# Performance work log

Hardware: AMD Instinct MI355X
Metric: run time of the kernel (lower is better)

Reference implementation:

```python
import jax, jax.numpy as jnp
import numpy as np

USER_NUM = 100000
ITEM_NUM = 50000
N = USER_NUM + ITEM_NUM
D = 64
NNZ = 2400000
B = 4096
NLEVEL = 3
LEAF = 32
HID = 256
NCLS = 2
NLAYERS = 2
EPS = 0.1
TAU = 0.2


def _l2norm(x, axis=-1):
    return x / jnp.clip(jnp.linalg.norm(x, axis=axis, keepdims=True), 1e-12)


def setup_inputs():
    key = jax.random.key(0)
    ks = jax.random.split(key, 32)
    def w(k, shape):
        fan = shape[-2] if len(shape) >= 2 else shape[-1]
        return jax.random.normal(k, shape, jnp.float32) / np.sqrt(fan)
    z = lambda *s: jnp.zeros(s, jnp.float32)
    return {
        "ego_emb": w(ks[0], (N, D)),
        "gc_w": w(ks[1], (NLAYERS, D, D)), "gc_b": z(NLAYERS, D),
        "bi_w": w(ks[2], (NLAYERS, D, D)), "bi_b": z(NLAYERS, D),
        "uh_w": w(ks[3], (NLEVEL, D, D)), "uh_b": z(NLEVEL, D),
        "ih_w": w(ks[4], (NLEVEL, D, D)), "ih_b": z(NLEVEL, D),
        "ud_w1": w(ks[5], (NLEVEL, D, HID)), "ud_b1": z(NLEVEL, HID),
        "ud_w2": w(ks[6], (NLEVEL, HID, LEAF)), "ud_b2": z(NLEVEL, LEAF),
        "id_w1": w(ks[7], (NLEVEL, D, HID)), "id_b1": z(NLEVEL, HID),
        "id_w2": w(ks[8], (NLEVEL, HID, LEAF)), "id_b2": z(NLEVEL, LEAF),
        "q_w": w(ks[9], (LEAF, LEAF)), "q_b": z(LEAF),
        "k_w": w(ks[10], (LEAF, LEAF)), "k_b": z(LEAF),
        "v_w": w(ks[11], (LEAF, LEAF)), "v_b": z(LEAF),
        "dg_w1": w(ks[12], (NLEVEL * LEAF, D)), "dg_b1": z(D),
        "dg_w2": w(ks[13], (D, D)), "dg_b2": z(D),
        "pr_w": w(ks[14], (D, NCLS)), "pr_b": z(NCLS),
        "adj_vals": jax.random.uniform(ks[15], (NNZ,), jnp.float32) / 16.0,
        "hier_skills": jax.random.uniform(ks[16], (B, NLEVEL * LEAF), jnp.float32),
        "user_id": jax.random.randint(ks[17], (B,), 0, USER_NUM),
        "item_id": jax.random.randint(ks[18], (B,), 0, ITEM_NUM),
        "adj_rows": jax.random.randint(ks[19], (NNZ,), 0, N),
        "adj_cols": jax.random.randint(ks[20], (NNZ,), 0, N),
    }


def _sam(x, q_w, q_b, k_w, k_b, v_w, v_b):
    # x: [B, S, d], single-head self-attention (n_heads=1)
    d = x.shape[-1]
    q = x @ q_w + q_b
    k = x @ k_w + k_b
    v = x @ v_w + v_b
    scores = jnp.einsum('bsd,btd->bst', q, k) / jnp.sqrt(jnp.float32(d))
    attn = jax.nn.softmax(scores, axis=-1)  # softmax over key axis t
    return jnp.einsum('bst,btd->bsd', attn, v)


def _cl_loss(v1, v2):
    n1 = _l2norm(v1)
    n2 = _l2norm(v2)
    pos = jnp.exp(jnp.sum(n1 * n2, -1) / TAU)
    ttl = jnp.sum(jnp.exp(n1 @ n2.T / TAU), axis=1)
    return jnp.mean(-jnp.log(pos / ttl))


def _cl_module(recs, key):
    # recs: [L, B, LEAF]
    noise = jax.random.uniform(key, recs.shape, recs.dtype)
    recs_new = recs + jnp.sign(recs) * _l2norm(noise) * EPS
    return jnp.mean(jax.vmap(_cl_loss)(recs, recs_new))


def reference(ego_emb, gc_w, gc_b, bi_w, bi_b, uh_w, uh_b, ih_w, ih_b,
              ud_w1, ud_b1, ud_w2, ud_b2, id_w1, id_b1, id_w2, id_b2,
              q_w, q_b, k_w, k_b, v_w, v_b, dg_w1, dg_b1, dg_w2, dg_b2,
              pr_w, pr_b, adj_vals, hier_skills, user_id, item_id,
              adj_rows, adj_cols):
    # ---- NGCF propagation: sparse adj matmul + bi-interaction ----
    E = ego_emb
    E_sum = ego_emb
    for l in range(NLAYERS):
        side = jax.ops.segment_sum(adj_vals[:, None] * E[adj_cols], adj_rows,
                                   num_segments=N)  # spmm(adj_norm, E)
        sum_e = jax.nn.leaky_relu(side @ gc_w[l] + gc_b[l])
        bi_e = jax.nn.leaky_relu((E * side) @ bi_w[l] + bi_b[l])
        E = _l2norm(sum_e + bi_e)  # dropout -> identity (eval)
        E_sum = E_sum + E
    ue = E_sum[:USER_NUM][user_id]   # [B, D]
    ie = E_sum[USER_NUM:][item_id]   # [B, D]
    # ---- hierarchy projections + disentangled encoders (stacked over levels) ----
    u_reps = jnp.tanh(jnp.einsum('bd,lde->lbe', ue, uh_w) + uh_b[:, None, :])
    i_reps = jnp.tanh(jnp.einsum('bd,lde->lbe', ie, ih_w) + ih_b[:, None, :])
    u_recs = jnp.einsum('lbh,lhk->lbk',
                        jnp.tanh(jnp.einsum('lbd,ldh->lbh', u_reps, ud_w1) + ud_b1[:, None, :]),
                        ud_w2) + ud_b2[:, None, :]  # [L, B, LEAF]
    i_recs = jnp.einsum('lbh,lhk->lbk',
                        jnp.tanh(jnp.einsum('lbd,ldh->lbh', i_reps, id_w1) + id_b1[:, None, :]),
                        id_w2) + id_b2[:, None, :]
    # ---- self-attention across levels ----
    u_att = _sam(u_recs.transpose(1, 0, 2), q_w, q_b, k_w, k_b, v_w, v_b)  # [B, L, LEAF]
    i_att = _sam(i_recs.transpose(1, 0, 2), q_w, q_b, k_w, k_b, v_w, v_b)
    # ---- contrastive losses (detached in original via torch.Tensor(...)) ----
    kc = jax.random.split(jax.random.key(42), 2)
    cl = _cl_module(u_att.transpose(1, 0, 2), kc[0]) + _cl_module(i_att.transpose(1, 0, 2), kc[1])
    cl = jax.lax.stop_gradient(cl)
    # ---- diagnosis head ----
    skills = hier_skills.reshape(B, NLEVEL, LEAF)
    diag = ((jax.nn.sigmoid(u_att) - jax.nn.sigmoid(i_att)) * skills).reshape(B, NLEVEL * LEAF)
    h = jnp.tanh(diag @ dg_w1 + dg_b1) @ dg_w2 + dg_b2  # dropout -> identity (eval)
    out = jax.nn.softmax(h @ pr_w + pr_b, axis=-1)
    return (out, cl)
```

## Files before the change

### kernel.cpp

```cpp
#include <hip/hip_runtime.h>
#include <stdint.h>
#include <math.h>

#define USER_N 100000
#define NODE_N 150000
#define DD 64
#define NNZE 2400000
#define BB 4096
#define NLV 3
#define LF 32
#define HALF_SZ 196608u
#define NTILE 586
#define NSUB 8
#define SCAP 1024
#define EPB 4096
#define LCAP 5120

typedef __attribute__((ext_vector_type(8))) short bf16x8;
typedef __attribute__((ext_vector_type(4))) float f32x4;
typedef __attribute__((ext_vector_type(2))) float f32x2;

#define XCC_ID_IMM 63508

__host__ __device__ inline void tf_block(uint32_t k0, uint32_t k1, uint32_t& x0, uint32_t& x1) {
  uint32_t ks[3] = {k0, k1, k0 ^ k1 ^ 0x1BD11BDAu};
  x0 += ks[0]; x1 += ks[1];
  const int R0[4] = {13, 15, 26, 6};
  const int R1[4] = {17, 29, 16, 24};
#pragma unroll
  for (int i = 0; i < 5; ++i) {
    const int* R = (i & 1) ? R1 : R0;
#pragma unroll
    for (int j = 0; j < 4; ++j) {
      x0 += x1;
      x1 = (x1 << R[j]) | (x1 >> (32 - R[j]));
      x1 ^= x0;
    }
    x0 += ks[(i + 1) % 3];
    x1 += ks[(i + 2) % 3] + (uint32_t)(i + 1);
  }
}

__device__ inline float tf_uniform(uint32_t ka, uint32_t kb, uint32_t m) {
  uint32_t x0, x1;
  bool first = m < HALF_SZ;
  if (first) { x0 = m; x1 = m + HALF_SZ; } else { x0 = m - HALF_SZ; x1 = m; }
  tf_block(ka, kb, x0, x1);
  uint32_t bits = first ? x0 : x1;
  return __uint_as_float((bits >> 9) | 0x3f800000u) - 1.0f;
}

__device__ inline unsigned short f2bf(float x) {
  uint32_t b = __float_as_uint(x);
  return (unsigned short)((b + 0x7FFFu + ((b >> 16) & 1u)) >> 16);
}

__device__ inline unsigned char f2fp8(float x) {
  return (unsigned char)(__builtin_amdgcn_cvt_pk_fp8_f32(x, x, 0, false) & 0xFF);
}

__device__ inline void fp8_fma(float4& acc, uint2 rec, uint32_t wrd) {
  float vv = __uint_as_float(rec.y);
  f32x2 lo = __builtin_amdgcn_cvt_pk_f32_fp8((int)wrd, false);
  f32x2 hi = __builtin_amdgcn_cvt_pk_f32_fp8((int)wrd, true);
  acc.x = fmaf(vv, lo.x, acc.x);
  acc.y = fmaf(vv, lo.y, acc.y);
  acc.z = fmaf(vv, hi.x, acc.z);
  acc.w = fmaf(vv, hi.y, acc.w);
}

__global__ __launch_bounds__(256) void k_init(
    const float* __restrict__ ego, uint32_t* __restrict__ E8,
    const float* __restrict__ uh_w, const float* __restrict__ ud_w1,
    const float* __restrict__ ud_w2, const float* __restrict__ ih_w,
    const float* __restrict__ id_w1, const float* __restrict__ id_w2,
    unsigned short* __restrict__ s1t, unsigned short* __restrict__ s2t,
    unsigned short* __restrict__ s3t) {
  if (blockIdx.x < 9375) {
    int i = blockIdx.x * 256 + threadIdx.x;
    float4 v = ((const float4*)ego)[i];
    int w01 = __builtin_amdgcn_cvt_pk_fp8_f32(v.x, v.y, 0, false);
    int w = __builtin_amdgcn_cvt_pk_fp8_f32(v.z, v.w, w01, true);
    E8[i] = (uint32_t)w;
    return;
  }
  int i = (blockIdx.x - 9375) * 256 + threadIdx.x;
  if (i < 24576) {
    int sl = i >> 12, r = i & 4095, e = r >> 6, d = r & 63;
    const float* src = (sl >= 3 ? ih_w : uh_w);
    int l = sl % 3;
    s1t[i] = f2bf(src[l * 4096 + d * 64 + e]);
  } else if (i < 24576 + 98304) {
    int j = i - 24576;
    int sl = j >> 14, r = j & 16383, e = r >> 6, d = r & 63;
    const float* src = (sl >= 3 ? id_w1 : ud_w1);
    int l = sl % 3;
    s2t[j] = f2bf(src[l * 16384 + d * 256 + e]);
  } else if (i < 172032) {
    int j = i - 24576 - 98304;
    int sl = j >> 13, r = j & 8191, e = r >> 8, d = r & 255;
    const float* src = (sl >= 3 ? id_w2 : ud_w2);
    int l = sl % 3;
    s3t[j] = f2bf(src[l * 8192 + d * 32 + e]);
  }
}

__global__ __launch_bounds__(256) void k_scatter_t(const int* __restrict__ rows,
                                                   const int* __restrict__ cols,
                                                   const float* __restrict__ vals,
                                                   int* __restrict__ cursor,
                                                   uint2* __restrict__ sedge_r) {
  __shared__ int cnt[NTILE];
  __shared__ int curs[NTILE];
  int t = threadIdx.x;
  for (int i = t; i < NTILE; i += 256) cnt[i] = 0;
  __syncthreads();
  int r[16];
  int ebase = blockIdx.x * EPB;
#pragma unroll
  for (int j = 0; j < 16; ++j) {
    int e = ebase + j * 256 + t;
    r[j] = (e < NNZE) ? rows[e] : -1;
    if (r[j] >= 0) atomicAdd(&cnt[r[j] >> 8], 1);
  }
  __syncthreads();
  unsigned myx = __builtin_amdgcn_s_getreg(XCC_ID_IMM) & (NSUB - 1);
  for (int i = t; i < NTILE; i += 256) {
    int c = cnt[i];
    curs[i] = c ? atomicAdd(&cursor[(i * NSUB + (int)myx) * 16], c) : 0;
  }
  __syncthreads();
#pragma unroll
  for (int j = 0; j < 16; ++j) {
    if (r[j] < 0) continue;
    int e = ebase + j * 256 + t;
    int tile = r[j] >> 8;
    uint2 rec = make_uint2((uint32_t)cols[e] | ((uint32_t)(r[j] & 255) << 18),
                           __float_as_uint(vals[e]));
    int p = atomicAdd(&curs[tile], 1);
    if (p < SCAP) {
      sedge_r[(size_t)(tile * NSUB + (int)myx) * SCAP + p] = rec;
    } else {
#pragma unroll 1
      for (int att = 1; att < NSUB; ++att) {
        int seg = tile * NSUB + (int)((myx + att) & (NSUB - 1));
        int p2 = atomicAdd(&cursor[seg * 16], 1);
        if (p2 < SCAP) { sedge_r[(size_t)seg * SCAP + p2] = rec; break; }
      }
    }
  }
}

__global__ __launch_bounds__(256) void k_sort_t(const uint2* __restrict__ sedge_r,
                                                const int* __restrict__ cursor,
                                                uint2* __restrict__ sedge,
                                                int* __restrict__ row_start) {
  __shared__ int hist[256], buf[256], curs[256];
  __shared__ int obase_s;
  __shared__ uint2 staged[LCAP];
  int t = threadIdx.x;
  int tile = blockIdx.x;
  if (t == 0) obase_s = 0;
  hist[t] = 0;
  __syncthreads();
  int ob = 0;
  for (int i = t; i < tile * NSUB; i += 256) {
    int c = cursor[i * 16];
    ob += (c < SCAP) ? c : SCAP;
  }
  if (ob) atomicAdd(&obase_s, ob);
  int segcnt[NSUB];
#pragma unroll
  for (int x = 0; x < NSUB; ++x) {
    int c = cursor[(tile * NSUB + x) * 16];
    segcnt[x] = (c < SCAP) ? c : SCAP;
  }
#pragma unroll 1
  for (int x = 0; x < NSUB; ++x) {
    const uint2* sp = sedge_r + (size_t)(tile * NSUB + x) * SCAP;
    for (int i = t; i < segcnt[x]; i += 256)
      atomicAdd(&hist[sp[i].x >> 18], 1);
  }
  __syncthreads();
  int obase = obase_s;
  int v = hist[t];
  buf[t] = v;
  __syncthreads();
  for (int off = 1; off < 256; off <<= 1) {
    int add = (t >= off) ? buf[t - off] : 0;
    __syncthreads();
    buf[t] += add;
    __syncthreads();
  }
  int total = buf[255];
  int excl = buf[t] - v;
  curs[t] = excl;
  int row = tile * 256 + t;
  if (row < NODE_N) row_start[row] = obase + excl;
  if (tile == NTILE - 1 && t == 0) row_start[NODE_N] = NNZE;
  __syncthreads();
#pragma unroll 1
  for (int x = 0; x < NSUB; ++x) {
    const uint2* sp = sedge_r + (size_t)(tile * NSUB + x) * SCAP;
    for (int i = t; i < segcnt[x]; i += 256) {
      uint2 rec = sp[i];
      int rl = rec.x >> 18;
      int p = atomicAdd(&curs[rl], 1);
      uint2 outrec = make_uint2(rec.x & 0x3FFFFu, rec.y);
      if (p < LCAP) staged[p] = outrec;
      else sedge[obase + p] = outrec;
    }
  }
  __syncthreads();
  int n = (total < LCAP) ? total : LCAP;
  for (int i = t; i < n; i += 256)
    sedge[obase + i] = staged[i];
}

__global__ __launch_bounds__(256) void k_spmm(const uint32_t* __restrict__ E8,
                                              const uint2* __restrict__ sedge,
                                              const int* __restrict__ row_start,
                                              unsigned short* __restrict__ side16,
                                              unsigned short* __restrict__ p16) {
  int r = blockIdx.x * 4 + (threadIdx.x >> 6);
  int lane = threadIdx.x & 63;
  int g = lane >> 4;
  int q = lane & 15;
  int rs = row_start[r], re = row_start[r + 1];
  float4 acc = make_float4(0.f, 0.f, 0.f, 0.f);
  int e = rs;
  for (; e + 16 <= re; e += 16) {
    uint2 e0 = sedge[e + g];
    uint2 e1 = sedge[e + 4 + g];
    uint2 e2 = sedge[e + 8 + g];
    uint2 e3 = sedge[e + 12 + g];
    uint32_t a0 = E8[(size_t)e0.x * 16 + q];
    uint32_t a1 = E8[(size_t)e1.x * 16 + q];
    uint32_t a2 = E8[(size_t)e2.x * 16 + q];
    uint32_t a3 = E8[(size_t)e3.x * 16 + q];
    fp8_fma(acc, e0, a0);
    fp8_fma(acc, e1, a1);
    fp8_fma(acc, e2, a2);
    fp8_fma(acc, e3, a3);
  }
  for (; e + 8 <= re; e += 8) {
    uint2 e0 = sedge[e + g];
    uint2 e1 = sedge[e + 4 + g];
    uint32_t a0 = E8[(size_t)e0.x * 16 + q];
    uint32_t a1 = E8[(size_t)e1.x * 16 + q];
    fp8_fma(acc, e0, a0);
    fp8_fma(acc, e1, a1);
  }
  for (; e + 4 <= re; e += 4) {
    uint2 e0 = sedge[e + g];
    uint32_t a0 = E8[(size_t)e0.x * 16 + q];
    fp8_fma(acc, e0, a0);
  }
  for (; e < re; ++e) {
    if (g == (e & 3)) {
      uint2 e0 = sedge[e];
      uint32_t a0 = E8[(size_t)e0.x * 16 + q];
      fp8_fma(acc, e0, a0);
    }
  }
#pragma unroll
  for (int off = 16; off <= 32; off <<= 1) {
    acc.x += __shfl_xor(acc.x, off, 64);
    acc.y += __shfl_xor(acc.y, off, 64);
    acc.z += __shfl_xor(acc.z, off, 64);
    acc.w += __shfl_xor(acc.w, off, 64);
  }
  if (g == 0) {
    uint32_t ew = E8[(size_t)r * 16 + q];
    f32x2 elo = __builtin_amdgcn_cvt_pk_f32_fp8((int)ew, false);
    f32x2 ehi = __builtin_amdgcn_cvt_pk_f32_fp8((int)ew, true);
    ushort4 s16, pp;
    s16.x = f2bf(acc.x); s16.y = f2bf(acc.y); s16.z = f2bf(acc.z); s16.w = f2bf(acc.w);
    pp.x = f2bf(acc.x * elo.x); pp.y = f2bf(acc.y * elo.y);
    pp.z = f2bf(acc.z * ehi.x); pp.w = f2bf(acc.w * ehi.y);
    *(ushort4*)&side16[(size_t)r * DD + q * 4] = s16;
    *(ushort4*)&p16[(size_t)r * DD + q * 4] = pp;
  }
}

__global__ __launch_bounds__(256) void k_transform(const float* __restrict__ gw,
                                                   const float* __restrict__ gb,
                                                   const float* __restrict__ bw,
                                                   const float* __restrict__ bb,
                                                   const unsigned short* __restrict__ side16,
                                                   const unsigned short* __restrict__ p16,
                                                   float* __restrict__ Eout,
                                                   unsigned char* __restrict__ E8b) {
  int t = threadIdx.x;
  int wv = t >> 6, lane = t & 63;
  int n = lane & 15, quad = lane >> 4;
  bf16x8 wg[4][2], wb[4][2];
  float gbl[4], bbl[4];
#pragma unroll
  for (int c = 0; c < 4; ++c) {
    gbl[c] = gb[c * 16 + n];
    bbl[c] = bb[c * 16 + n];
#pragma unroll
    for (int h = 0; h < 2; ++h) {
#pragma unroll
      for (int j = 0; j < 8; ++j) {
        int k = h * 32 + quad * 8 + j;
        wg[c][h][j] = (short)f2bf(gw[k * 64 + c * 16 + n]);
        wb[c][h][j] = (short)f2bf(bw[k * 64 + c * 16 + n]);
      }
    }
  }
  const f32x4 z = {0.f, 0.f, 0.f, 0.f};
  for (int tile = blockIdx.x * 4 + wv; tile < NODE_N / 16; tile += gridDim.x * 4) {
    int i0 = tile * 16;
    bf16x8 as0 = *(const bf16x8*)&side16[(size_t)(i0 + n) * DD + quad * 8];
    bf16x8 as1 = *(const bf16x8*)&side16[(size_t)(i0 + n) * DD + 32 + quad * 8];
    bf16x8 ap0 = *(const bf16x8*)&p16[(size_t)(i0 + n) * DD + quad * 8];
    bf16x8 ap1 = *(const bf16x8*)&p16[(size_t)(i0 + n) * DD + 32 + quad * 8];
    float v[4][4];
    float sq0 = 0.f, sq1 = 0.f, sq2 = 0.f, sq3 = 0.f;
#pragma unroll
    for (int c = 0; c < 4; ++c) {
      f32x4 ag = __builtin_amdgcn_mfma_f32_16x16x32_bf16(as0, wg[c][0], z, 0, 0, 0);
      ag = __builtin_amdgcn_mfma_f32_16x16x32_bf16(as1, wg[c][1], ag, 0, 0, 0);
      f32x4 ab = __builtin_amdgcn_mfma_f32_16x16x32_bf16(ap0, wb[c][0], z, 0, 0, 0);
      ab = __builtin_amdgcn_mfma_f32_16x16x32_bf16(ap1, wb[c][1], ab, 0, 0, 0);
#pragma unroll
      for (int r = 0; r < 4; ++r) {
        float a1 = ag[r] + gbl[c];
        a1 = (a1 > 0.f) ? a1 : 0.01f * a1;
        float a2 = ab[r] + bbl[c];
        a2 = (a2 > 0.f) ? a2 : 0.01f * a2;
        float vv = a1 + a2;
        v[c][r] = vv;
        if (r == 0) sq0 += vv * vv;
        else if (r == 1) sq1 += vv * vv;
        else if (r == 2) sq2 += vv * vv;
        else sq3 += vv * vv;
      }
    }
#pragma unroll
    for (int off = 1; off < 16; off <<= 1) {
      sq0 += __shfl_xor(sq0, off, 64);
      sq1 += __shfl_xor(sq1, off, 64);
      sq2 += __shfl_xor(sq2, off, 64);
      sq3 += __shfl_xor(sq3, off, 64);
    }
    float inv0 = 1.f / fmaxf(sqrtf(sq0), 1e-12f);
    float inv1 = 1.f / fmaxf(sqrtf(sq1), 1e-12f);
    float inv2 = 1.f / fmaxf(sqrtf(sq2), 1e-12f);
    float inv3 = 1.f / fmaxf(sqrtf(sq3), 1e-12f);
#pragma unroll
    for (int c = 0; c < 4; ++c) {
      float vn0 = v[c][0] * inv0;
      float vn1 = v[c][1] * inv1;
      float vn2 = v[c][2] * inv2;
      float vn3 = v[c][3] * inv3;
      size_t o0 = (size_t)(i0 + quad * 4 + 0) * DD + c * 16 + n;
      size_t o1 = o0 + DD, o2 = o1 + DD, o3 = o2 + DD;
      Eout[o0] = vn0; Eout[o1] = vn1; Eout[o2] = vn2; Eout[o3] = vn3;
      E8b[o0] = f2fp8(vn0); E8b[o1] = f2fp8(vn1);
      E8b[o2] = f2fp8(vn2); E8b[o3] = f2fp8(vn3);
    }
  }
}

__global__ __launch_bounds__(128) void k_gather(const float* __restrict__ ego,
                                                const float* __restrict__ E1,
                                                const float* __restrict__ E2,
                                                const int* __restrict__ uid,
                                                const int* __restrict__ iid,
                                                unsigned short* __restrict__ ue16,
                                                unsigned short* __restrict__ ie16) {
  int b = blockIdx.x, t = threadIdx.x;
  if (t < 64) {
    size_t o = (size_t)uid[b] * 64 + t;
    ue16[(size_t)b * 64 + t] = f2bf(ego[o] + E1[o] + E2[o]);
  } else {
    int d = t - 64;
    size_t o = (size_t)(USER_N + iid[b]) * 64 + d;
    ie16[(size_t)b * 64 + d] = f2bf(ego[o] + E1[o] + E2[o]);
  }
}

__global__ __launch_bounds__(256) void k_encoder5(
    const unsigned short* __restrict__ ue16, const unsigned short* __restrict__ ie16,
    const unsigned short* __restrict__ s1t, const unsigned short* __restrict__ s2t,
    const unsigned short* __restrict__ s3t,
    const float* __restrict__ uh_b, const float* __restrict__ ud_b1,
    const float* __restrict__ ud_b2, const float* __restrict__ ih_b,
    const float* __restrict__ id_b1, const float* __restrict__ id_b2,
    float* __restrict__ recs_u, float* __restrict__ recs_i) {
  __shared__ unsigned short R1[32][64];
  __shared__ unsigned short T[32][256];
  int t = threadIdx.x;
  int w = t >> 6, lane = t & 63;
  int n = lane & 15, quad = lane >> 4;
  int trow = w & 1;
  int cg = w >> 1;
  int r0 = blockIdx.x * 32;
  int l = blockIdx.y, side = blockIdx.z;
  int sl = side * 3 + l;
  const unsigned short* x16 = side ? ie16 : ue16;
  const float* hb = side ? ih_b : uh_b;
  const float* bb1 = side ? id_b1 : ud_b1;
  const float* bb2 = side ? id_b2 : ud_b2;
  float* recs = side ? recs_i : recs_u;
  const f32x4 z = {0.f, 0.f, 0.f, 0.f};

  {
    const unsigned short* xr = &x16[(size_t)(r0 + trow * 16 + n) * 64];
    bf16x8 a0 = *(const bf16x8*)&xr[quad * 8];
    bf16x8 a1 = *(const bf16x8*)&xr[32 + quad * 8];
    const unsigned short* Wt = s1t + (size_t)sl * 4096;
#pragma unroll
    for (int cc = 0; cc < 2; ++cc) {
      int cb = cg * 2 + cc;
      bf16x8 wb0 = *(const bf16x8*)&Wt[(size_t)(cb * 16 + n) * 64 + quad * 8];
      bf16x8 wb1 = *(const bf16x8*)&Wt[(size_t)(cb * 16 + n) * 64 + 32 + quad * 8];
      f32x4 acc = __builtin_amdgcn_mfma_f32_16x16x32_bf16(a0, wb0, z, 0, 0, 0);
      acc = __builtin_amdgcn_mfma_f32_16x16x32_bf16(a1, wb1, acc, 0, 0, 0);
      float bias = hb[l * 64 + cb * 16 + n];
#pragma unroll
      for (int r = 0; r < 4; ++r)
        R1[trow * 16 + quad * 4 + r][cb * 16 + n] = f2bf(tanhf(acc[r] + bias));
    }
  }
  __syncthreads();

  {
    bf16x8 a0 = *(const bf16x8*)&R1[trow * 16 + n][quad * 8];
    bf16x8 a1 = *(const bf16x8*)&R1[trow * 16 + n][32 + quad * 8];
    const unsigned short* Wt = s2t + (size_t)sl * 16384;
#pragma unroll
    for (int cc = 0; cc < 8; ++cc) {
      int cb = cg * 8 + cc;
      bf16x8 wb0 = *(const bf16x8*)&Wt[(size_t)(cb * 16 + n) * 64 + quad * 8];
      bf16x8 wb1 = *(const bf16x8*)&Wt[(size_t)(cb * 16 + n) * 64 + 32 + quad * 8];
      f32x4 acc = __builtin_amdgcn_mfma_f32_16x16x32_bf16(a0, wb0, z, 0, 0, 0);
      acc = __builtin_amdgcn_mfma_f32_16x16x32_bf16(a1, wb1, acc, 0, 0, 0);
      float bias = bb1[l * 256 + cb * 16 + n];
#pragma unroll
      for (int r = 0; r < 4; ++r)
        T[trow * 16 + quad * 4 + r][cb * 16 + n] = f2bf(tanhf(acc[r] + bias));
    }
  }
  __syncthreads();

  {
    const unsigned short* Wt = s3t + (size_t)sl * 8192;
    f32x4 acc = z;
#pragma unroll
    for (int h = 0; h < 8; ++h) {
      bf16x8 a = *(const bf16x8*)&T[trow * 16 + n][h * 32 + quad * 8];
      bf16x8 b = *(const bf16x8*)&Wt[(size_t)(cg * 16 + n) * 256 + h * 32 + quad * 8];
      acc = __builtin_amdgcn_mfma_f32_16x16x32_bf16(a, b, acc, 0, 0, 0);
    }
    float bias = bb2[l * 32 + cg * 16 + n];
#pragma unroll
    for (int r = 0; r < 4; ++r)
      recs[((size_t)l * BB + (r0 + trow * 16 + quad * 4 + r)) * 32 + cg * 16 + n] =
          acc[r] + bias;
  }
}

__global__ __launch_bounds__(256) void k_attn(const float* __restrict__ recs_u,
                                              const float* __restrict__ recs_i,
                                              const float* __restrict__ qw, const float* __restrict__ qb,
                                              const float* __restrict__ kw, const float* __restrict__ kb,
                                              const float* __restrict__ vw, const float* __restrict__ vb,
                                              float* __restrict__ att_u,
                                              float* __restrict__ att_i) {
  const float* recs = blockIdx.y ? recs_i : recs_u;
  float* att = blockIdx.y ? att_i : att_u;
  int t = threadIdx.x;
  int b = blockIdx.x * 8 + (t >> 5);
  int d = t & 31;
  float x0 = recs[((size_t)0 * BB + b) * 32 + d];
  float x1 = recs[((size_t)1 * BB + b) * 32 + d];
  float x2 = recs[((size_t)2 * BB + b) * 32 + d];
  float q0 = qb[d], q1 = q0, q2 = q0;
  float c0 = kb[d], c1 = c0, c2 = c0;
  float v0 = vb[d], v1 = v0, v2 = v0;
#pragma unroll 4
  for (int kk = 0; kk < 32; ++kk) {
    float xa = __shfl(x0, kk, 32);
    float xb = __shfl(x1, kk, 32);
    float xc = __shfl(x2, kk, 32);
    float wq = qw[kk * 32 + d], wk = kw[kk * 32 + d], wv = vw[kk * 32 + d];
    q0 += xa * wq; q1 += xb * wq; q2 += xc * wq;
    c0 += xa * wk; c1 += xb * wk; c2 += xc * wk;
    v0 += xa * wv; v1 += xb * wv; v2 += xc * wv;
  }
  float qs[3] = {q0, q1, q2}, ks[3] = {c0, c1, c2}, vs[3] = {v0, v1, v2};
  float sc[3][3];
#pragma unroll
  for (int s = 0; s < 3; ++s)
#pragma unroll
    for (int u = 0; u < 3; ++u) {
      float p = qs[s] * ks[u];
#pragma unroll
      for (int off = 16; off; off >>= 1) p += __shfl_xor(p, off, 32);
      sc[s][u] = p * 0.17677669529663687f;
    }
#pragma unroll
  for (int s = 0; s < 3; ++s) {
    float m = fmaxf(sc[s][0], fmaxf(sc[s][1], sc[s][2]));
    float e0 = __expf(sc[s][0] - m), e1 = __expf(sc[s][1] - m), e2 = __expf(sc[s][2] - m);
    float inv = 1.f / (e0 + e1 + e2);
    att[(size_t)b * 96 + s * 32 + d] = (e0 * vs[0] + e1 * vs[1] + e2 * vs[2]) * inv;
  }
}

__global__ __launch_bounds__(256) void k_noise(const float* __restrict__ att_u,
                                               const float* __restrict__ att_i,
                                               uint32_t ku0, uint32_t ku1, uint32_t ki0, uint32_t ki1,
                                               unsigned short* __restrict__ n1b,
                                               unsigned short* __restrict__ n2b,
                                               float* __restrict__ posdot) {
  int t = threadIdx.x;
  int g = blockIdx.x * 8 + (t >> 5);
  int k = t & 31;
  int side = g / (NLV * BB);
  int rem = g - side * (NLV * BB);
  int l = rem >> 12;
  int b = rem & 4095;
  const float* att = side ? att_i : att_u;
  uint32_t ka = side ? ki0 : ku0;
  uint32_t kb = side ? ki1 : ku1;
  float r = att[(size_t)b * 96 + l * 32 + k];
  float ss = r * r;
#pragma unroll
  for (int off = 16; off; off >>= 1) ss += __shfl_xor(ss, off, 32);
  float v1 = r / fmaxf(sqrtf(ss), 1e-12f);
  uint32_t m = ((uint32_t)(l * BB + b)) * 32u + (uint32_t)k;
  float u = tf_uniform(ka, kb, m);
  float us = u * u;
#pragma unroll
  for (int off = 16; off; off >>= 1) us += __shfl_xor(us, off, 32);
  float un = u / fmaxf(sqrtf(us), 1e-12f);
  float sgn = (r > 0.f) ? 1.f : ((r < 0.f) ? -1.f : 0.f);
  float rn = r + sgn * un * 0.1f;
  float s2 = rn * rn;
#pragma unroll
  for (int off = 16; off; off >>= 1) s2 += __shfl_xor(s2, off, 32);
  float v2 = rn / fmaxf(sqrtf(s2), 1e-12f);
  float pd = v1 * v2;
#pragma unroll
  for (int off = 16; off; off >>= 1) pd += __shfl_xor(pd, off, 32);
  size_t o = (size_t)g * 32 + k;
  n1b[o] = f2bf(v1);
  n2b[o] = f2bf(v2);
  if (k == 0) posdot[g] = pd;
}

__global__ __launch_bounds__(256) void k_ttl(const unsigned short* __restrict__ n1b,
                                             const unsigned short* __restrict__ n2b,
                                             float* __restrict__ ttl) {
  int t = threadIdx.x;
  int wv = t >> 6, lane = t & 63;
  int sl = blockIdx.x >> 6;
  int istripe = blockIdx.x & 63;
  int i0 = istripe * 64 + wv * 16;
  const unsigned short* ab = n1b + (size_t)sl * BB * 32;
  const unsigned short* bb = n2b + (size_t)sl * BB * 32;
  int m = lane & 15, quad = lane >> 4;
  bf16x8 afrag = *(const bf16x8*)&ab[(size_t)(i0 + m) * 32 + quad * 8];
  float r0a = 0.f, r1a = 0.f, r2a = 0.f, r3a = 0.f;
  f32x4 z = {0.f, 0.f, 0.f, 0.f};
  for (int jt = 0; jt < 256; jt += 4) {
    bf16x8 b0 = *(const bf16x8*)&bb[((size_t)((jt + 0) * 16 + m)) * 32 + quad * 8];
    bf16x8 b1 = *(const bf16x8*)&bb[((size_t)((jt + 1) * 16 + m)) * 32 + quad * 8];
    bf16x8 b2 = *(const bf16x8*)&bb[((size_t)((jt + 2) * 16 + m)) * 32 + quad * 8];
    bf16x8 b3 = *(const bf16x8*)&bb[((size_t)((jt + 3) * 16 + m)) * 32 + quad * 8];
    f32x4 s0 = __builtin_amdgcn_mfma_f32_16x16x32_bf16(afrag, b0, z, 0, 0, 0);
    f32x4 s1 = __builtin_amdgcn_mfma_f32_16x16x32_bf16(afrag, b1, z, 0, 0, 0);
    f32x4 s2 = __builtin_amdgcn_mfma_f32_16x16x32_bf16(afrag, b2, z, 0, 0, 0);
    f32x4 s3 = __builtin_amdgcn_mfma_f32_16x16x32_bf16(afrag, b3, z, 0, 0, 0);
    r0a += __expf(s0.x * 5.f) + __expf(s1.x * 5.f) + __expf(s2.x * 5.f) + __expf(s3.x * 5.f);
    r1a += __expf(s0.y * 5.f) + __expf(s1.y * 5.f) + __expf(s2.y * 5.f) + __expf(s3.y * 5.f);
    r2a += __expf(s0.z * 5.f) + __expf(s1.z * 5.f) + __expf(s2.z * 5.f) + __expf(s3.z * 5.f);
    r3a += __expf(s0.w * 5.f) + __expf(s1.w * 5.f) + __expf(s2.w * 5.f) + __expf(s3.w * 5.f);
  }
#pragma unroll
  for (int off = 1; off < 16; off <<= 1) {
    r0a += __shfl_xor(r0a, off, 64);
    r1a += __shfl_xor(r1a, off, 64);
    r2a += __shfl_xor(r2a, off, 64);
    r3a += __shfl_xor(r3a, off, 64);
  }
  if (m == 0) {
    int rbase = sl * BB + i0 + quad * 4;
    ttl[rbase + 0] = r0a;
    ttl[rbase + 1] = r1a;
    ttl[rbase + 2] = r2a;
    ttl[rbase + 3] = r3a;
  }
}

__global__ __launch_bounds__(1024) void k_clred(const float* __restrict__ ttl,
                                                const float* __restrict__ posdot,
                                                float* __restrict__ outp) {
  __shared__ float red[1024];
  int t = threadIdx.x;
  float a = 0.f;
  for (int idx = t; idx < 6 * BB; idx += 1024)
    a += logf(ttl[idx]) - posdot[idx] * 5.0f;
  red[t] = a;
  __syncthreads();
  for (int off = 512; off; off >>= 1) {
    if (t < off) red[t] += red[t + off];
    __syncthreads();
  }
  if (t == 0) outp[2 * BB] = red[0] * (1.f / 12288.f);
}

__global__ __launch_bounds__(256) void k_head(const float* __restrict__ att_u,
                                              const float* __restrict__ att_i,
                                              const float* __restrict__ skills,
                                              const float* __restrict__ w1, const float* __restrict__ b1,
                                              const float* __restrict__ w2, const float* __restrict__ b2,
                                              const float* __restrict__ pw, const float* __restrict__ pb,
                                              float* __restrict__ outp) {
  __shared__ float diag[4][96], t1[4][64];
  int t = threadIdx.x;
  int w = t >> 6, lane = t & 63;
  int b = blockIdx.x * 4 + w;
  for (int j = lane; j < 96; j += 64) {
    float su = 1.f / (1.f + __expf(-att_u[(size_t)b * 96 + j]));
    float si = 1.f / (1.f + __expf(-att_i[(size_t)b * 96 + j]));
    diag[w][j] = (su - si) * skills[(size_t)b * 96 + j];
  }
  __syncthreads();
  float a = b1[lane];
#pragma unroll 8
  for (int j = 0; j < 96; ++j) a += diag[w][j] * w1[j * 64 + lane];
  t1[w][lane] = tanhf(a);
  __syncthreads();
  float h = b2[lane];
#pragma unroll 8
  for (int kk = 0; kk < 64; ++kk) h += t1[w][kk] * w2[kk * 64 + lane];
  float p0 = h * pw[lane * 2 + 0];
  float p1 = h * pw[lane * 2 + 1];
#pragma unroll
  for (int off = 32; off; off >>= 1) {
    p0 += __shfl_xor(p0, off, 64);
    p1 += __shfl_xor(p1, off, 64);
  }
  if (lane == 0) {
    float l0 = p0 + pb[0], l1 = p1 + pb[1];
    float m = fmaxf(l0, l1);
    float e0 = __expf(l0 - m), e1 = __expf(l1 - m);
    float inv = 1.f / (e0 + e1);
    outp[(size_t)b * 2 + 0] = e0 * inv;
    outp[(size_t)b * 2 + 1] = e1 * inv;
  }
}

extern "C" void kernel_launch(void* const* d_in, const int* in_sizes, int n_in,
                              void* d_out, int out_size, void* d_ws, size_t ws_size,
                              hipStream_t stream) {
  const float* ego    = (const float*)d_in[0];
  const float* gc_w   = (const float*)d_in[1];
  const float* gc_b   = (const float*)d_in[2];
  const float* bi_w   = (const float*)d_in[3];
  const float* bi_b   = (const float*)d_in[4];
  const float* uh_w   = (const float*)d_in[5];
  const float* uh_b   = (const float*)d_in[6];
  const float* ih_w   = (const float*)d_in[7];
  const float* ih_b   = (const float*)d_in[8];
  const float* ud_w1  = (const float*)d_in[9];
  const float* ud_b1  = (const float*)d_in[10];
  const float* ud_w2  = (const float*)d_in[11];
  const float* ud_b2  = (const float*)d_in[12];
  const float* id_w1  = (const float*)d_in[13];
  const float* id_b1  = (const float*)d_in[14];
  const float* id_w2  = (const float*)d_in[15];
  const float* id_b2  = (const float*)d_in[16];
  const float* q_w    = (const float*)d_in[17];
  const float* q_b    = (const float*)d_in[18];
  const float* k_w    = (const float*)d_in[19];
  const float* k_b    = (const float*)d_in[20];
  const float* v_w    = (const float*)d_in[21];
  const float* v_b    = (const float*)d_in[22];
  const float* dg_w1  = (const float*)d_in[23];
  const float* dg_b1  = (const float*)d_in[24];
  const float* dg_w2  = (const float*)d_in[25];
  const float* dg_b2  = (const float*)d_in[26];
  const float* pr_w   = (const float*)d_in[27];
  const float* pr_b   = (const float*)d_in[28];
  const float* adj_vals = (const float*)d_in[29];
  const float* skills = (const float*)d_in[30];
  const int* user_id  = (const int*)d_in[31];
  const int* item_id  = (const int*)d_in[32];
  const int* adj_rows = (const int*)d_in[33];
  const int* adj_cols = (const int*)d_in[34];
  float* outp = (float*)d_out;

  char* w = (char*)d_ws;
  auto alloc = [&](size_t bytes) -> char* {
    char* p = w;
    w += (bytes + 255) & ~(size_t)255;
    return p;
  };
  float* E1     = (float*)alloc((size_t)NODE_N * DD * 4);
  float* E2     = (float*)alloc((size_t)NODE_N * DD * 4);
  uint32_t* E8  = (uint32_t*)alloc((size_t)NODE_N * DD);
  unsigned short* side16 = (unsigned short*)alloc((size_t)NODE_N * DD * 2);
  unsigned short* p16    = (unsigned short*)alloc((size_t)NODE_N * DD * 2);
  uint2* sedge_r= (uint2*)alloc((size_t)NTILE * NSUB * SCAP * 8);
  uint2* sedge  = (uint2*)alloc((size_t)NNZE * 8);
  int*   cursor = (int*)  alloc((size_t)NTILE * NSUB * 16 * 4);
  int*   row_start = (int*)alloc((size_t)(NODE_N + 1) * 4);
  float* posdot = (float*)alloc((size_t)6 * BB * 4);
  float* ttl    = (float*)alloc((size_t)6 * BB * 4);
  unsigned short* s1t = (unsigned short*)alloc((size_t)24576 * 2);
  unsigned short* s2t = (unsigned short*)alloc((size_t)98304 * 2);
  unsigned short* s3t = (unsigned short*)alloc((size_t)49152 * 2);

  char* ap = (char*)sedge_r;
  auto alias = [&](size_t bytes) -> char* {
    char* p = ap;
    ap += (bytes + 255) & ~(size_t)255;
    return p;
  };
  unsigned short* ue16 = (unsigned short*)alias((size_t)BB * 64 * 2);
  unsigned short* ie16 = (unsigned short*)alias((size_t)BB * 64 * 2);
  float* recs_u = (float*)alias((size_t)NLV * BB * 32 * 4);
  float* recs_i = (float*)alias((size_t)NLV * BB * 32 * 4);
  float* att_u  = (float*)alias((size_t)BB * 96 * 4);
  float* att_i  = (float*)alias((size_t)BB * 96 * 4);
  unsigned short* n1b = (unsigned short*)alias((size_t)6 * BB * 32 * 2);
  unsigned short* n2b = (unsigned short*)alias((size_t)6 * BB * 32 * 2);

  uint32_t a0 = 0, a1 = 2, b0 = 1, b1 = 3;
  tf_block(0u, 42u, a0, a1);
  tf_block(0u, 42u, b0, b1);
  uint32_t ku0 = a0, ku1 = b0;
  uint32_t ki0 = a1, ki1 = b1;

  (void)hipMemsetAsync(cursor, 0, (size_t)NTILE * NSUB * 16 * 4, stream);

  k_init<<<9375 + 672, 256, 0, stream>>>(ego, E8, uh_w, ud_w1, ud_w2,
                                         ih_w, id_w1, id_w2, s1t, s2t, s3t);
  k_scatter_t<<<(NNZE + EPB - 1) / EPB, 256, 0, stream>>>(adj_rows, adj_cols, adj_vals,
                                                          cursor, sedge_r);
  k_sort_t<<<NTILE, 256, 0, stream>>>(sedge_r, cursor, sedge, row_start);

  float* Ebufs[2] = {E1, E2};
  for (int l = 0; l < 2; ++l) {
    k_spmm<<<37500, 256, 0, stream>>>(E8, sedge, row_start, side16, p16);
    k_transform<<<1172, 256, 0, stream>>>(gc_w + l * 4096, gc_b + l * 64,
                                          bi_w + l * 4096, bi_b + l * 64,
                                          side16, p16, Ebufs[l], (unsigned char*)E8);
  }

  k_gather<<<4096, 128, 0, stream>>>(ego, E1, E2, user_id, item_id, ue16, ie16);

  dim3 ge(128, 3, 2);
  k_encoder5<<<ge, 256, 0, stream>>>(ue16, ie16, s1t, s2t, s3t,
                                     uh_b, ud_b1, ud_b2, ih_b, id_b1, id_b2,
                                     recs_u, recs_i);

  dim3 ga(512, 2);
  k_attn<<<ga, 256, 0, stream>>>(recs_u, recs_i, q_w, q_b, k_w, k_b, v_w, v_b,
                                 att_u, att_i);

  k_noise<<<3072, 256, 0, stream>>>(att_u, att_i, ku0, ku1, ki0, ki1, n1b, n2b, posdot);

  k_ttl<<<384, 256, 0, stream>>>(n1b, n2b, ttl);
  k_clred<<<1, 1024, 0, stream>>>(ttl, posdot, outp);

  k_head<<<1024, 256, 0, stream>>>(att_u, att_i, skills, dg_w1, dg_b1, dg_w2, dg_b2,
                                   pr_w, pr_b, outp);
}
```

Measured before the change: 540.6 us.

## Stage scatter records in LDS sorted by tile for coalesced global writes

The edge scatter kernel now ranks each edge within its tile bin during counting, builds an exclusive prefix sum of the bin counts in shared memory, and stages records contiguously per tile in LDS. It then writes the records out in bin order, so consecutive threads write consecutive addresses within each tile segment instead of scattering randomly. This aims to cut uncoalesced global stores, at the cost of about 40KB of LDS per block (lower occupancy) and an extra scan with several barriers.

```diff
diff --git a/kernel.cpp b/kernel.cpp
--- a/kernel.cpp
+++ b/kernel.cpp
@@ -111,23 +111,46 @@
                                                    int* __restrict__ cursor,
                                                    uint2* __restrict__ sedge_r) {
   __shared__ int cnt[NTILE];
-  __shared__ int curs[NTILE];
+  __shared__ int binbase[NTILE];
+  __shared__ int gbase[NTILE];
+  __shared__ int partial[256];
+  __shared__ uint2 staged[EPB];
+  __shared__ unsigned short tileof[EPB];
   int t = threadIdx.x;
   for (int i = t; i < NTILE; i += 256) cnt[i] = 0;
   __syncthreads();
-  int r[16];
   int ebase = blockIdx.x * EPB;
+  int r[16], rk[16];
 #pragma unroll
   for (int j = 0; j < 16; ++j) {
     int e = ebase + j * 256 + t;
     r[j] = (e < NNZE) ? rows[e] : -1;
-    if (r[j] >= 0) atomicAdd(&cnt[r[j] >> 8], 1);
-  }
-  __syncthreads();
+    rk[j] = (r[j] >= 0) ? atomicAdd(&cnt[r[j] >> 8], 1) : 0;
+  }
+  __syncthreads();
+  int b0 = t * 3;
+  int own = (b0 < NTILE) ? ((NTILE - b0 < 3) ? (NTILE - b0) : 3) : 0;
+  int s0 = 0;
+  for (int k = 0; k < own; ++k) s0 += cnt[b0 + k];
+  partial[t] = s0;
+  __syncthreads();
+  for (int off = 1; off < 256; off <<= 1) {
+    int add = (t >= off) ? partial[t - off] : 0;
+    __syncthreads();
+    partial[t] += add;
+    __syncthreads();
+  }
+  int excl = partial[t] - s0;
   unsigned myx = __builtin_amdgcn_s_getreg(XCC_ID_IMM) & (NSUB - 1);
-  for (int i = t; i < NTILE; i += 256) {
-    int c = cnt[i];
-    curs[i] = c ? atomicAdd(&cursor[(i * NSUB + (int)myx) * 16], c) : 0;
+  {
+    int run = excl;
+    for (int k = 0; k < own; ++k) {
+      int b = b0 + k;
+      int c = cnt[b];
+      binbase[b] = run;
+      gbase[b] = c ? atomicAdd(&cursor[(b * NSUB + (int)myx) * 16], c) : 0;
+      run += c;
+    }
   }
   __syncthreads();
 #pragma unroll
@@ -135,9 +158,19 @@
     if (r[j] < 0) continue;
     int e = ebase + j * 256 + t;
     int tile = r[j] >> 8;
-    uint2 rec = make_uint2((uint32_t)cols[e] | ((uint32_t)(r[j] & 255) << 18),
-                           __float_as_uint(vals[e]));
-    int p = atomicAdd(&curs[tile], 1);
+    int pos = binbase[tile] + rk[j];
+    staged[pos] = make_uint2((uint32_t)cols[e] | ((uint32_t)(r[j] & 255) << 18),
+                             __float_as_uint(vals[e]));
+    tileof[pos] = (unsigned short)tile;
+  }
+  __syncthreads();
+  int nrec = NNZE - ebase;
+  if (nrec > EPB) nrec = EPB;
+  for (int i = t; i < nrec; i += 256) {
+    int tile = tileof[i];
+    int q = i - binbase[tile];
+    int p = gbase[tile] + q;
+    uint2 rec = staged[i];
     if (p < SCAP) {
       sedge_r[(size_t)(tile * NSUB + (int)myx) * SCAP + p] = rec;
     } else {
```

After: 524.6 us. 3.0% less time.
